# Kernel optimization log

Measured on AMD Instinct MI355X. Metric: run time of the kernel, lower is better.

The kernel has to match this reference:

```python
import jax, jax.numpy as jnp
import numpy as np

B, S, D, H = 4, 2048, 1024, 16
DK = D // H
THETA = 10000.0


def setup_inputs() -> dict:
    key = jax.random.key(0)
    ks = jax.random.split(key, 5)
    std = (2.0 / (D + D)) ** 0.5  # Linear init std (distribution differs from trunc-normal; math identical)
    x = jax.random.normal(ks[0], (B, S, D), dtype=jnp.float32)
    wq = jax.random.normal(ks[1], (D, D), dtype=jnp.float32) * std
    wk = jax.random.normal(ks[2], (D, D), dtype=jnp.float32) * std
    wv = jax.random.normal(ks[3], (D, D), dtype=jnp.float32) * std
    wo = jax.random.normal(ks[4], (D, D), dtype=jnp.float32) * std
    mask = jnp.tril(jnp.ones((S, S), dtype=bool))  # causal
    return {"x": x, "mask": mask, "wq": wq, "wk": wk, "wv": wv, "wo": wo}


def _rope(t):
    # t: [b, h, s, dk]; interleaved pairs (even, odd)
    s = t.shape[-2]
    inv_freq = THETA ** (-jnp.arange(0, DK, 2, dtype=jnp.float32) / DK)  # [dk/2]
    ang = jnp.arange(s, dtype=jnp.float32)[:, None] * inv_freq[None, :]  # [s, dk/2]
    cos = jnp.cos(ang)[None, None, :, :]
    sin = jnp.sin(ang)[None, None, :, :]
    x1 = t[..., 0::2]
    x2 = t[..., 1::2]
    rot = jnp.stack([x1 * cos - x2 * sin, x1 * sin + x2 * cos], axis=-1)
    return rot.reshape(t.shape)


def reference(x, mask, wq, wk, wv, wo):
    b, s, d = x.shape
    def heads(w):
        return jnp.einsum('bsd,ed->bse', x, w).reshape(b, s, H, DK).transpose(0, 2, 1, 3)
    q = _rope(heads(wq))
    k = _rope(heads(wk))
    v = heads(wv)
    scores = jnp.einsum('bhqd,bhkd->bhqk', q, k) / (DK ** 0.5)
    scores = jnp.where(mask, scores, -jnp.inf)
    attn = jax.nn.softmax(scores, axis=-1)
    out = jnp.einsum('bhqk,bhkd->bhqd', attn, v)
    out = out.transpose(0, 2, 1, 3).reshape(b, s, d)
    return jnp.einsum('bsd,ed->bse', out, wo)
```

## Files before the change

### kernel.cpp

```cpp
#include <hip/hip_runtime.h>

constexpr int Bc = 4, Sc = 2048, Dc = 1024, Hc = 16, DKc = 64;
constexpr int Mc = Bc * Sc;

typedef __bf16 bf16x8 __attribute__((ext_vector_type(8)));
typedef float f32x4 __attribute__((ext_vector_type(4)));
typedef unsigned short ush;

#define DEVI __device__ __forceinline__

DEVI ush bf(float f) { return __builtin_bit_cast(ush, (__bf16)f); }

DEVI void ld_lds16(const void* g, void* l) {
    __builtin_amdgcn_global_load_lds(
        (const __attribute__((address_space(1))) unsigned int*)g,
        (__attribute__((address_space(3))) unsigned int*)l,
        16, 0, 0);
}

constexpr unsigned CVT_BLOCKS = 6144;
constexpr unsigned TAB_BLOCKS = 32;

__global__ __launch_bounds__(256) void cvt_all(
    const float* __restrict__ x,  const float* __restrict__ wq,
    const float* __restrict__ wk, const float* __restrict__ wv,
    const float* __restrict__ wo, ush* __restrict__ dst,
    float2* __restrict__ csn)
{
    if (blockIdx.x >= CVT_BLOCKS) {
        int t = (int)(blockIdx.x - CVT_BLOCKS) * 256 + threadIdx.x;
#pragma unroll
        for (int i = 0; i < 8; i++) {
            int idx = t * 8 + i;
            int s = idx >> 5, p = idx & 31;
            float ang = (float)s * exp2f(-(float)p * 0.4152410118609203f);
            csn[idx] = make_float2(cosf(ang), sinf(ang));
        }
        return;
    }
    size_t t = ((size_t)blockIdx.x * 256 + threadIdx.x) * 8;
    const float* src; size_t loc;
    const size_t NX = (size_t)Mc * Dc;
    if (t < NX) { src = x; loc = t; }
    else {
        size_t u = t - NX;
        int wi = (int)(u >> 20);
        src = (wi == 0) ? wq : ((wi == 1) ? wk : ((wi == 2) ? wv : wo));
        loc = u & 1048575u;
    }
    float4 a = *(const float4*)(src + loc);
    float4 b = *(const float4*)(src + loc + 4);
    union { ush u[8]; float4 v; } o;
    o.u[0] = bf(a.x); o.u[1] = bf(a.y); o.u[2] = bf(a.z); o.u[3] = bf(a.w);
    o.u[4] = bf(b.x); o.u[5] = bf(b.y); o.u[6] = bf(b.z); o.u[7] = bf(b.w);
    *(float4*)(dst + t) = o.v;
}

template<int MODE>
__global__ __launch_bounds__(256) void gemm_bf(
    const ush* __restrict__ A,
    const ush* __restrict__ W0, const ush* __restrict__ W1,
    const ush* __restrict__ W2,
    ush* __restrict__ Oq, ush* __restrict__ Ok, ush* __restrict__ Ovt,
    float* __restrict__ Of, const float2* __restrict__ csn)
{
    __shared__ ush sA[128 * 64];
    __shared__ ush sB[128 * 64];

    const int xcd = (int)blockIdx.x;
    const int u = (int)blockIdx.y + 64 * (int)blockIdx.z;
    const int z = (MODE == 0) ? (u >> 6) : 0;
    const int w = u & 63;
    const int m0 = (xcd * 8 + (w >> 3)) * 128;
    const int n0 = (w & 7) * 128;

    const ush* W = (z == 0) ? W0 : ((z == 1) ? W1 : W2);

    const int tid = threadIdx.x;
    const int wv = tid >> 6;
    const int ln = tid & 63;
    const int lr = ln & 15;
    const int lq = ln >> 4;
    const int wm = (wv & 1) * 64;
    const int wn = (wv >> 1) * 64;
    const int rL = ln >> 3;
    const int cSw = ((ln & 7) ^ rL) * 8;
    const int ca0 = lq ^ (ln & 7);

    f32x4 acc[4][4] = {};
    const bool swp = (MODE == 0) && (z == 2);

    for (int kt = 0; kt < 1024; kt += 64) {
        __syncthreads();
#pragma unroll
        for (int i = 0; i < 4; i++) {
            int chunk = wv * 4 + i;
            int rr = chunk * 8 + rL;
            ld_lds16(&A[(size_t)(m0 + rr) * 1024 + kt + cSw], &sA[chunk * 512]);
            ld_lds16(&W[(size_t)(n0 + rr) * 1024 + kt + cSw], &sB[chunk * 512]);
        }
        __syncthreads();
#pragma unroll
        for (int ks = 0; ks < 2; ks++) {
            const int cf = (ca0 ^ (ks << 2)) << 3;
            bf16x8 af[4], bfr[4];
#pragma unroll
            for (int t = 0; t < 4; t++) {
                af[t]  = *(const bf16x8*)(&sA[(wm + t * 16 + lr) * 64 + cf]);
                bfr[t] = *(const bf16x8*)(&sB[(wn + t * 16 + lr) * 64 + cf]);
            }
            __builtin_amdgcn_s_setprio(1);
            if (!swp) {
#pragma unroll
                for (int mt = 0; mt < 4; mt++)
#pragma unroll
                    for (int nt = 0; nt < 4; nt++)
                        acc[mt][nt] = __builtin_amdgcn_mfma_f32_16x16x32_bf16(
                            af[mt], bfr[nt], acc[mt][nt], 0, 0, 0);
            } else {
#pragma unroll
                for (int mt = 0; mt < 4; mt++)
#pragma unroll
                    for (int nt = 0; nt < 4; nt++)
                        acc[mt][nt] = __builtin_amdgcn_mfma_f32_16x16x32_bf16(
                            bfr[mt], af[nt], acc[mt][nt], 0, 0, 0);
            }
            __builtin_amdgcn_s_setprio(0);
        }
    }

    ush* Oqk = (z == 0) ? Oq : Ok;
#pragma unroll
    for (int mt = 0; mt < 4; mt++) {
#pragma unroll
        for (int nt = 0; nt < 4; nt++) {
#pragma unroll
            for (int r = 0; r < 4; r++) {
                float v = acc[mt][nt][r];
                if (MODE == 1) {
                    int m = m0 + wm + mt * 16 + lq * 4 + r;
                    int n = n0 + wn + nt * 16 + lr;
                    Of[(size_t)m * 1024 + n] = v;
                } else if (swp) {
                    int n = n0 + wn + mt * 16 + lq * 4 + r;
                    int m = m0 + wm + nt * 16 + lr;
                    Ovt[((size_t)((m >> 11) * Hc + (n >> 6)) * DKc + (n & 63)) * Sc
                        + (m & (Sc - 1))] = bf(v);
                } else {
                    int m = m0 + wm + mt * 16 + lq * 4 + r;
                    int n = n0 + wn + nt * 16 + lr;
                    float part = __shfl_xor(v, 1);
                    int dk = n & 63, s = m & (Sc - 1);
                    float2 cs = csn[(s << 5) + (dk >> 1)];
                    float res = (dk & 1) ? (part * cs.y + v * cs.x)
                                         : (v * cs.x - part * cs.y);
                    if (z == 0) res *= 0.18033688011112042f;
                    Oqk[((size_t)((m >> 11) * Hc + (n >> 6)) * Sc + s) * DKc + dk] = bf(res);
                }
            }
        }
    }
}

__global__ __launch_bounds__(512, 4) void attn_k(
    const ush* __restrict__ Q, const ush* __restrict__ Kr,
    const ush* __restrict__ Vt, ush* __restrict__ O)
{
    __shared__ ush kbuf[64 * 64];
    __shared__ ush vbuf[64 * 64];
    __shared__ ush pbuf[8][16 * 76];

    const int head = (int)blockIdx.x * 8 + ((int)blockIdx.y >> 3);
    const int qp   = (int)blockIdx.y & 7;
    const int tid = threadIdx.x;
    const int wv = tid >> 6;
    const int ln = tid & 63;
    const int lr = ln & 15;
    const int lq = ln >> 4;
    const size_t hoff = (size_t)head * Sc * DKc;
    const int rS = tid >> 3;
    const int c8 = tid & 7;
    const int cS = c8 * 8;
    const int cW = ((c8 ^ (rS & 7)) * 8);
    const int cw0 = ((lq ^ (lr & 7)) * 8);

#define LOADKV(ktv, kk, vv) {                                                \
        int kb_ = (ktv) * 64;                                                \
        kk = *(const float4*)(&Kr[hoff + (size_t)(kb_ + rS) * DKc + cS]);    \
        vv = *(const float4*)(&Vt[hoff + (size_t)rS * Sc + kb_ + cS]); }

#define WRITEKV(kk, vv) {                                                    \
        *(float4*)(&kbuf[rS * 64 + cW]) = kk;                                \
        *(float4*)(&vbuf[rS * 64 + cW]) = vv; }

#define COMPUTE(ktv) {                                                       \
        const int kb = (ktv) * 64;                                           \
        f32x4 sc[4];                                                         \
        __builtin_amdgcn_s_setprio(1);                                       \
        _Pragma("unroll")                                                    \
        for (int nt = 0; nt < 4; nt++) {                                     \
            const ush* kr_ = &kbuf[(nt * 16 + lr) * 64];                     \
            bf16x8 bk0 = *(const bf16x8*)(kr_ + cw0);                        \
            bf16x8 bk1 = *(const bf16x8*)(kr_ + (cw0 ^ 32));                 \
            f32x4 cc = {};                                                   \
            cc = __builtin_amdgcn_mfma_f32_16x16x32_bf16(aq0, bk0, cc, 0, 0, 0); \
            cc = __builtin_amdgcn_mfma_f32_16x16x32_bf16(aq1, bk1, cc, 0, 0, 0); \
            sc[nt] = cc;                                                     \
        }                                                                    \
        __builtin_amdgcn_s_setprio(0);                                       \
        const int rowq = qbase + wv * 16 + lq * 4;                           \
        const bool needmask = (kb + 63 > qbase + wv * 16);                   \
        _Pragma("unroll")                                                    \
        for (int nt = 0; nt < 4; nt++) {                                     \
            int col = kb + nt * 16 + lr;                                     \
            _Pragma("unroll")                                                \
            for (int r = 0; r < 4; r++) {                                    \
                float v = sc[nt][r];                                         \
                if (needmask && col > rowq + r) v = -1e30f;                  \
                float p = exp2f(v);                                          \
                sc[nt][r] = p;                                               \
                rs[r] += p;                                                  \
            }                                                                \
        }                                                                    \
        {                                                                    \
            ush* pb = pbuf[wv];                                              \
            _Pragma("unroll")                                                \
            for (int nt = 0; nt < 4; nt++)                                   \
                _Pragma("unroll")                                            \
                for (int r = 0; r < 4; r++)                                  \
                    pb[(lq * 4 + r) * 76 + nt * 16 + lr] = bf(sc[nt][r]);    \
            __builtin_amdgcn_s_setprio(1);                                   \
            _Pragma("unroll")                                                \
            for (int ks = 0; ks < 2; ks++) {                                 \
                bf16x8 ap = *(const bf16x8*)(&pb[lr * 76 + ks * 32 + lq * 8]); \
                _Pragma("unroll")                                            \
                for (int nt = 0; nt < 4; nt++) {                             \
                    bf16x8 bv = *(const bf16x8*)(&vbuf[(nt * 16 + lr) * 64   \
                                                       + (cw0 ^ (ks * 32))]); \
                    oacc[nt] = __builtin_amdgcn_mfma_f32_16x16x32_bf16(      \
                        ap, bv, oacc[nt], 0, 0, 0);                          \
                }                                                            \
            }                                                                \
            __builtin_amdgcn_s_setprio(0);                                   \
        }                                                                    \
    }

    for (int half = 0; half < 2; half++) {
        const int qt = half ? (15 - qp) : qp;
        const int qbase = qt * 128;
        const int kmax = 2 * qt + 2;

        bf16x8 aq0, aq1;
        {
            int row = qbase + wv * 16 + lr;
            const ush* qp_ = &Q[hoff + (size_t)row * DKc + lq * 8];
            aq0 = *(const bf16x8*)(qp_);
            aq1 = *(const bf16x8*)(qp_ + 32);
        }

        f32x4 oacc[4] = {};
        float rs[4] = {};

        float4 ka, va, kb2, vb2;

        LOADKV(0, ka, va);
        int kt = 0;
        while (true) {
            __syncthreads();
            WRITEKV(ka, va);
            __syncthreads();
            if (kt + 1 < kmax) LOADKV(kt + 1, kb2, vb2);
            COMPUTE(kt);
            kt++;
            if (kt >= kmax) break;
            __syncthreads();
            WRITEKV(kb2, vb2);
            __syncthreads();
            if (kt + 1 < kmax) LOADKV(kt + 1, ka, va);
            COMPUTE(kt);
            kt++;
            if (kt >= kmax) break;
        }

        const int b = head >> 4, h = head & 15;
#pragma unroll
        for (int r = 0; r < 4; r++) {
            float l = rs[r];
#pragma unroll
            for (int d = 1; d < 16; d <<= 1) l += __shfl_xor(l, d);
            float inv = 1.0f / l;
            int srow = qbase + wv * 16 + lq * 4 + r;
#pragma unroll
            for (int nt = 0; nt < 4; nt++) {
                int e = h * 64 + nt * 16 + lr;
                O[((size_t)(b * Sc + srow)) * Dc + e] = bf(oacc[nt][r] * inv);
            }
        }
    }
#undef LOADKV
#undef WRITEKV
#undef COMPUTE
}

extern "C" void kernel_launch(void* const* d_in, const int* in_sizes, int n_in,
                              void* d_out, int out_size, void* d_ws, size_t ws_size,
                              hipStream_t stream)
{
    (void)in_sizes; (void)n_in; (void)out_size; (void)ws_size;
    const float* x  = (const float*)d_in[0];
    const float* wq = (const float*)d_in[2];
    const float* wk = (const float*)d_in[3];
    const float* wv = (const float*)d_in[4];
    const float* wo = (const float*)d_in[5];

    const size_t N = (size_t)Mc * Dc;
    const size_t NW = (size_t)Dc * Dc;

    ush* xh  = (ush*)d_ws;
    ush* wqh = xh  + N;
    ush* wkh = wqh + NW;
    ush* wvh = wkh + NW;
    ush* woh = wvh + NW;
    ush* vt  = woh + NW;
    ush* ows = vt  + N;
    float2* csn = (float2*)(ows + N);
    ush* qd = (ush*)d_out;
    ush* kd = qd + N;

    cvt_all<<<dim3(CVT_BLOCKS + TAB_BLOCKS), 256, 0, stream>>>(
        x, wq, wk, wv, wo, xh, csn);
    gemm_bf<0><<<dim3(8, 64, 3), 256, 0, stream>>>(
        xh, wqh, wkh, wvh, qd, kd, vt, nullptr, csn);
    attn_k<<<dim3(8, 64), 512, 0, stream>>>(qd, kd, vt, ows);
    gemm_bf<1><<<dim3(8, 64, 1), 256, 0, stream>>>(
        ows, woh, woh, woh, nullptr, nullptr, nullptr, (float*)d_out, csn);
}
```

Baseline: 322.8 us.

## Double-buffer LDS tiles in projection GEMM to overlap loads with MFMA

The bf16 GEMM now keeps two LDS buffers for the A and W tiles and issues the global-to-LDS loads for the next K step before computing the current one. Explicit vmcnt waits and s_barrier calls replace the two __syncthreads per iteration, so load latency can overlap with MFMA work. This doubles LDS use to 64KB per block, which may reduce occupancy. It also depends on the hand-written waitcnt counts matching the 8 outstanding loads per stage.

```diff
diff --git a/kernel.cpp b/kernel.cpp
--- a/kernel.cpp
+++ b/kernel.cpp
@@ -64,8 +64,8 @@
     ush* __restrict__ Oq, ush* __restrict__ Ok, ush* __restrict__ Ovt,
     float* __restrict__ Of, const float2* __restrict__ csn)
 {
-    __shared__ ush sA[128 * 64];
-    __shared__ ush sB[128 * 64];
+    __shared__ ush sA[2][128 * 64];
+    __shared__ ush sB[2][128 * 64];
 
     const int xcd = (int)blockIdx.x;
     const int u = (int)blockIdx.y + 64 * (int)blockIdx.z;
@@ -90,44 +90,66 @@
     f32x4 acc[4][4] = {};
     const bool swp = (MODE == 0) && (z == 2);
 
+#define STAGE(buf, ktv) {                                                     \
+        _Pragma("unroll")                                                     \
+        for (int i = 0; i < 4; i++) {                                         \
+            int chunk = wv * 4 + i;                   \
+            int rr = chunk * 8 + rL;                                          \
+            ld_lds16(&A[(size_t)(m0 + rr) * 1024 + (ktv) + cSw],              \
+                     &sA[buf][chunk * 512]);                                  \
+            ld_lds16(&W[(size_t)(n0 + rr) * 1024 + (ktv) + cSw],              \
+                     &sB[buf][chunk * 512]);                                  \
+        } }
+
+#define COMPUTE(b) {                                                          \
+        const ush* pA = sA[b]; const ush* pB = sB[b];                         \
+        _Pragma("unroll")                                                     \
+        for (int ks = 0; ks < 2; ks++) {                                      \
+            const int cf = (ca0 ^ (ks << 2)) << 3;                            \
+            bf16x8 af[4], bfr[4];                                             \
+            _Pragma("unroll")                                                 \
+            for (int t = 0; t < 4; t++) {                                     \
+                af[t]  = *(const bf16x8*)(&pA[(wm + t * 16 + lr) * 64 + cf]); \
+                bfr[t] = *(const bf16x8*)(&pB[(wn + t * 16 + lr) * 64 + cf]); \
+            }                                                                 \
+            __builtin_amdgcn_s_setprio(1);                                    \
+            if (!swp) {                                                       \
+                _Pragma("unroll")                                             \
+                for (int mt = 0; mt < 4; mt++)                                \
+                    _Pragma("unroll")                                         \
+                    for (int nt = 0; nt < 4; nt++)                            \
+                        acc[mt][nt] = __builtin_amdgcn_mfma_f32_16x16x32_bf16(\
+                            af[mt], bfr[nt], acc[mt][nt], 0, 0, 0);           \
+            } else {                                                          \
+                _Pragma("unroll")                                             \
+                for (int mt = 0; mt < 4; mt++)                                \
+                    _Pragma("unroll")                                         \
+                    for (int nt = 0; nt < 4; nt++)                            \
+                        acc[mt][nt] = __builtin_amdgcn_mfma_f32_16x16x32_bf16(\
+                            bfr[mt], af[nt], acc[mt][nt], 0, 0, 0);           \
+            }                                                                 \
+            __builtin_amdgcn_s_setprio(0);                                    \
+        } }
+
+    STAGE(0, 0);
+
     for (int kt = 0; kt < 1024; kt += 64) {
-        __syncthreads();
-#pragma unroll
-        for (int i = 0; i < 4; i++) {
-            int chunk = wv * 4 + i;
-            int rr = chunk * 8 + rL;
-            ld_lds16(&A[(size_t)(m0 + rr) * 1024 + kt + cSw], &sA[chunk * 512]);
-            ld_lds16(&W[(size_t)(n0 + rr) * 1024 + kt + cSw], &sB[chunk * 512]);
-        }
-        __syncthreads();
-#pragma unroll
-        for (int ks = 0; ks < 2; ks++) {
-            const int cf = (ca0 ^ (ks << 2)) << 3;
-            bf16x8 af[4], bfr[4];
-#pragma unroll
-            for (int t = 0; t < 4; t++) {
-                af[t]  = *(const bf16x8*)(&sA[(wm + t * 16 + lr) * 64 + cf]);
-                bfr[t] = *(const bf16x8*)(&sB[(wn + t * 16 + lr) * 64 + cf]);
-            }
-            __builtin_amdgcn_s_setprio(1);
-            if (!swp) {
-#pragma unroll
-                for (int mt = 0; mt < 4; mt++)
-#pragma unroll
-                    for (int nt = 0; nt < 4; nt++)
-                        acc[mt][nt] = __builtin_amdgcn_mfma_f32_16x16x32_bf16(
-                            af[mt], bfr[nt], acc[mt][nt], 0, 0, 0);
-            } else {
-#pragma unroll
-                for (int mt = 0; mt < 4; mt++)
-#pragma unroll
-                    for (int nt = 0; nt < 4; nt++)
-                        acc[mt][nt] = __builtin_amdgcn_mfma_f32_16x16x32_bf16(
-                            bfr[mt], af[nt], acc[mt][nt], 0, 0, 0);
-            }
-            __builtin_amdgcn_s_setprio(0);
-        }
-    }
+        const int cb = (kt >> 6) & 1;
+        if (kt + 64 < 1024) {
+            STAGE(cb ^ 1, kt + 64);
+            asm volatile("s_waitcnt vmcnt(8)" ::: "memory");
+        } else {
+            asm volatile("s_waitcnt vmcnt(0)" ::: "memory");
+        }
+        __builtin_amdgcn_sched_barrier(0);
+        __builtin_amdgcn_s_barrier();
+        COMPUTE(cb);
+        asm volatile("s_waitcnt lgkmcnt(0)" ::: "memory");
+        __builtin_amdgcn_sched_barrier(0);
+        __builtin_amdgcn_s_barrier();
+    }
+#undef STAGE
+#undef COMPUTE
 
     ush* Oqk = (z == 0) ? Oq : Ok;
 #pragma unroll
```

Result: no change. 323.3 us (+0.2%).
